# Performance work log

Measured on AMD Instinct MI355X. Metric: run time of the kernel, lower is better.

## Reference

```python
import jax, jax.numpy as jnp
import numpy as np

B, D, C = 16384, 1024, 2048

def setup_inputs() -> dict:
    key = jax.random.key(0)
    k1, k2 = jax.random.split(key)
    x = jax.random.normal(k1, (B, D), dtype=jnp.float32)
    # kaiming_normal_ with nonlinearity='relu': std = sqrt(2 / fan_in)
    W = jax.random.normal(k2, (C, D), dtype=jnp.float32) * jnp.sqrt(2.0 / D)
    return {"x": x, "W": W, "task_id": 0}

def reference(x, W, task_id):
    # Original: -(x[:, :, None] - W.T[None, :, :])**2 .mean(1)  -> [B, C]
    # Algebraic rewrite: -(||x||^2/D - 2*x.W^T/D + ||w||^2/D)
    d = jnp.asarray(x.shape[1], x.dtype)
    x2 = jnp.sum(x * x, axis=1, keepdims=True) / d          # [B, 1]
    w2 = jnp.sum(W * W, axis=1) / d                          # [C]
    cross = jnp.einsum('bd,cd->bc', x, W) * (2.0 / d)        # [B, C]
    return cross - x2 - w2[None, :]
```

## Files before the change

kernel.cpp:

```cpp
#include <hip/hip_runtime.h>
#include <hip/hip_bf16.h>
#include <stdint.h>

#define B_ROWS 16384
#define D_DIM  1024
#define C_DIM  2048

#define BM 128
#define BN 128
#define BK 64

typedef short bf16x8 __attribute__((ext_vector_type(8)));
typedef float f32x4  __attribute__((ext_vector_type(4)));

__global__ __launch_bounds__(256) void cvt_norm_all(
        const float* __restrict__ x, const float* __restrict__ W,
        ushort* __restrict__ xb, ushort* __restrict__ wb,
        float* __restrict__ x2, float* __restrict__ w2) {
    const int blk = blockIdx.x;
    const float* src; ushort* dst; float* norm; int row;
    if (blk < B_ROWS) { src = x; dst = xb; norm = x2; row = blk; }
    else              { src = W; dst = wb; norm = w2; row = blk - B_ROWS; }

    const int t = threadIdx.x;
    const float4 v = ((const float4*)(src + (size_t)row * D_DIM))[t];
    float s = v.x * v.x + v.y * v.y + v.z * v.z + v.w * v.w;

    ushort4 u;
    __hip_bfloat16 h;
    h = __float2bfloat16(v.x); u.x = *(const ushort*)&h;
    h = __float2bfloat16(v.y); u.y = *(const ushort*)&h;
    h = __float2bfloat16(v.z); u.z = *(const ushort*)&h;
    h = __float2bfloat16(v.w); u.w = *(const ushort*)&h;
    ((ushort4*)(dst + (size_t)row * D_DIM))[t] = u;

    #pragma unroll
    for (int o = 32; o > 0; o >>= 1) s += __shfl_down(s, o, 64);
    __shared__ float red[4];
    if ((t & 63) == 0) red[t >> 6] = s;
    __syncthreads();
    if (t == 0)
        norm[row] = (red[0] + red[1] + red[2] + red[3]) * (1.0f / (float)D_DIM);
}

__global__ __launch_bounds__(256) void gemm_epilogue(
        const ushort* __restrict__ xb, const ushort* __restrict__ wb,
        const float* __restrict__ x2, const float* __restrict__ w2,
        float* __restrict__ out) {
    __shared__ ushort As[BM * BK];
    __shared__ ushort Bs[BN * BK];

    const int tid  = threadIdx.x;
    const int lane = tid & 63;
    const int nT   = C_DIM / BN;
    const int per  = (B_ROWS / BM) * nT / 8;
    const int wid  = (blockIdx.x & 7) * per + (blockIdx.x >> 3);
    const int mBase = (wid / nT) * BM;
    const int nBase = (wid % nT) * BN;

    const int waveM = ((tid >> 6) >> 1) * 64;
    const int waveN = ((tid >> 6) & 1) * 64;

    f32x4 acc[4][4];
    #pragma unroll
    for (int mi = 0; mi < 4; ++mi)
        #pragma unroll
        for (int ni = 0; ni < 4; ++ni)
            acc[mi][ni] = (f32x4){0.f, 0.f, 0.f, 0.f};

    const ushort* aG = xb + (size_t)mBase * D_DIM;
    const ushort* bG = wb + (size_t)nBase * D_DIM;

    const int rsel = lane & 15;
    const int quad = lane >> 4;
    const int rk   = rsel & 7;

    for (int kt = 0; kt < D_DIM; kt += BK) {
        #pragma unroll
        for (int j = 0; j < 4; ++j) {
            const int c    = j * 256 + tid;
            const int row  = c >> 3;
            const int ksrc = (c & 7) ^ (row & 7);
            const int ldsb = (j * 256 + (tid & 192)) * 8;
            __builtin_amdgcn_global_load_lds(
                (const __attribute__((address_space(1))) void*)(aG + (size_t)row * D_DIM + kt + ksrc * 8),
                (__attribute__((address_space(3))) void*)(As + ldsb), 16, 0, 0);
            __builtin_amdgcn_global_load_lds(
                (const __attribute__((address_space(1))) void*)(bG + (size_t)row * D_DIM + kt + ksrc * 8),
                (__attribute__((address_space(3))) void*)(Bs + ldsb), 16, 0, 0);
        }
        __syncthreads();

        #pragma unroll
        for (int ks = 0; ks < 2; ++ks) {
            const int kph = ((ks * 4 + quad) ^ rk) * 8;
            bf16x8 a[4], b[4];
            #pragma unroll
            for (int mi = 0; mi < 4; ++mi)
                a[mi] = *(const bf16x8*)(As + (waveM + mi * 16 + rsel) * BK + kph);
            #pragma unroll
            for (int ni = 0; ni < 4; ++ni)
                b[ni] = *(const bf16x8*)(Bs + (waveN + ni * 16 + rsel) * BK + kph);
            #pragma unroll
            for (int mi = 0; mi < 4; ++mi)
                #pragma unroll
                for (int ni = 0; ni < 4; ++ni)
                    acc[mi][ni] = __builtin_amdgcn_mfma_f32_16x16x32_bf16(
                        a[mi], b[ni], acc[mi][ni], 0, 0, 0);
        }
        __syncthreads();
    }

    const float scale = 2.0f / (float)D_DIM;
    const int col0 = nBase + waveN + rsel;
    const int row0 = mBase + waveM + quad * 4;

    float x2r[4][4];
    #pragma unroll
    for (int mi = 0; mi < 4; ++mi)
        #pragma unroll
        for (int r = 0; r < 4; ++r)
            x2r[mi][r] = x2[row0 + mi * 16 + r];

    #pragma unroll
    for (int ni = 0; ni < 4; ++ni) {
        const int c = col0 + ni * 16;
        const float wc = w2[c];
        #pragma unroll
        for (int mi = 0; mi < 4; ++mi) {
            #pragma unroll
            for (int r = 0; r < 4; ++r) {
                const int rr = row0 + mi * 16 + r;
                out[(size_t)rr * C_DIM + c] = acc[mi][ni][r] * scale - x2r[mi][r] - wc;
            }
        }
    }
}

extern "C" void kernel_launch(void* const* d_in, const int* in_sizes, int n_in,
                              void* d_out, int out_size, void* d_ws, size_t ws_size,
                              hipStream_t stream) {
    const float* x = (const float*)d_in[0];
    const float* W = (const float*)d_in[1];
    float* out = (float*)d_out;

    char* ws = (char*)d_ws;
    ushort* xb = (ushort*)ws;
    ushort* wb = (ushort*)(ws + (size_t)B_ROWS * D_DIM * sizeof(ushort));
    float*  x2 = (float*)(ws + (size_t)(B_ROWS + C_DIM) * D_DIM * sizeof(ushort));
    float*  w2 = x2 + B_ROWS;

    cvt_norm_all<<<B_ROWS + C_DIM, 256, 0, stream>>>(x, W, xb, wb, x2, w2);
    gemm_epilogue<<<(B_ROWS / BM) * (C_DIM / BN), 256, 0, stream>>>(xb, wb, x2, w2, out);
}
```

Before: 267.3 us.

## Pre-pack operands into MFMA fragment layout and drop LDS from GEMM

The conversion kernel now writes x and W as bf16 in a tile-packed layout that matches the MFMA operand fragments, and accumulates row norms with atomics after a memset. The GEMM reads fragments straight from global memory into registers with double-buffered prefetch. This removes shared-memory staging and barriers. In exchange it loses LDS reuse across waves, so each wave fetches its own A/B fragments and L2 traffic goes up. It also adds an extra memset launch and atomic norm accumulation.

```diff
diff --git a/kernel.cpp b/kernel.cpp
--- a/kernel.cpp
+++ b/kernel.cpp
@@ -5,61 +5,65 @@
 #define B_ROWS 16384
 #define D_DIM  1024
 #define C_DIM  2048
-
-#define BM 128
-#define BN 128
-#define BK 64
+#define MT_TOT (B_ROWS / 16)
+#define NT_TOT (C_DIM  / 16)
+#define KT_TOT (D_DIM  / 32)
 
 typedef short bf16x8 __attribute__((ext_vector_type(8)));
 typedef float f32x4  __attribute__((ext_vector_type(4)));
 
-__global__ __launch_bounds__(256) void cvt_norm_all(
+__global__ __launch_bounds__(256) void pack_norm(
         const float* __restrict__ x, const float* __restrict__ W,
-        ushort* __restrict__ xb, ushort* __restrict__ wb,
+        ushort* __restrict__ Apk, ushort* __restrict__ Bpk,
         float* __restrict__ x2, float* __restrict__ w2) {
-    const int blk = blockIdx.x;
-    const float* src; ushort* dst; float* norm; int row;
-    if (blk < B_ROWS) { src = x; dst = xb; norm = x2; row = blk; }
-    else              { src = W; dst = wb; norm = w2; row = blk - B_ROWS; }
+    int chunk = blockIdx.x * 4 + (threadIdx.x >> 6);
+    const int lane = threadIdx.x & 63;
+    const int XCH = MT_TOT * KT_TOT;
+    const float* src; ushort* dst; float* norm;
+    if (chunk < XCH) { src = x; dst = Apk; norm = x2; }
+    else             { src = W; dst = Bpk; norm = w2; chunk -= XCH; }
+    const int tile = chunk >> 5;
+    const int kt   = chunk & 31;
 
-    const int t = threadIdx.x;
-    const float4 v = ((const float4*)(src + (size_t)row * D_DIM))[t];
-    float s = v.x * v.x + v.y * v.y + v.z * v.z + v.w * v.w;
+    const int row = tile * 16 + (lane & 15);
+    const int k0  = kt * 32 + (lane >> 4) * 8;
+    const float4 v0 = *(const float4*)(src + (size_t)row * D_DIM + k0);
+    const float4 v1 = *(const float4*)(src + (size_t)row * D_DIM + k0 + 4);
+    float s = v0.x*v0.x + v0.y*v0.y + v0.z*v0.z + v0.w*v0.w
+            + v1.x*v1.x + v1.y*v1.y + v1.z*v1.z + v1.w*v1.w;
 
-    ushort4 u;
-    __hip_bfloat16 h;
-    h = __float2bfloat16(v.x); u.x = *(const ushort*)&h;
-    h = __float2bfloat16(v.y); u.y = *(const ushort*)&h;
-    h = __float2bfloat16(v.z); u.z = *(const ushort*)&h;
-    h = __float2bfloat16(v.w); u.w = *(const ushort*)&h;
-    ((ushort4*)(dst + (size_t)row * D_DIM))[t] = u;
+    ushort u[8]; __hip_bfloat16 h;
+    h = __float2bfloat16(v0.x); u[0] = *(const ushort*)&h;
+    h = __float2bfloat16(v0.y); u[1] = *(const ushort*)&h;
+    h = __float2bfloat16(v0.z); u[2] = *(const ushort*)&h;
+    h = __float2bfloat16(v0.w); u[3] = *(const ushort*)&h;
+    h = __float2bfloat16(v1.x); u[4] = *(const ushort*)&h;
+    h = __float2bfloat16(v1.y); u[5] = *(const ushort*)&h;
+    h = __float2bfloat16(v1.z); u[6] = *(const ushort*)&h;
+    h = __float2bfloat16(v1.w); u[7] = *(const ushort*)&h;
+    *(bf16x8*)(dst + ((size_t)chunk * 64 + lane) * 8) = *(const bf16x8*)u;
 
-    #pragma unroll
-    for (int o = 32; o > 0; o >>= 1) s += __shfl_down(s, o, 64);
-    __shared__ float red[4];
-    if ((t & 63) == 0) red[t >> 6] = s;
-    __syncthreads();
-    if (t == 0)
-        norm[row] = (red[0] + red[1] + red[2] + red[3]) * (1.0f / (float)D_DIM);
+    s += __shfl_xor(s, 16, 64);
+    s += __shfl_xor(s, 32, 64);
+    if (lane < 16) atomicAdd(norm + tile * 16 + lane, s * (1.0f / (float)D_DIM));
 }
 
-__global__ __launch_bounds__(256) void gemm_epilogue(
-        const ushort* __restrict__ xb, const ushort* __restrict__ wb,
+__global__ __launch_bounds__(256, 3) void gemm_flat(
+        const ushort* __restrict__ Apk, const ushort* __restrict__ Bpk,
         const float* __restrict__ x2, const float* __restrict__ w2,
         float* __restrict__ out) {
-    __shared__ ushort As[BM * BK];
-    __shared__ ushort Bs[BN * BK];
-
     const int tid  = threadIdx.x;
     const int lane = tid & 63;
-    const int nT   = C_DIM / BN;
-    const int per  = (B_ROWS / BM) * nT / 8;
-    const int wid  = (blockIdx.x & 7) * per + (blockIdx.x >> 3);
-    const int mBase = (wid / nT) * BM;
-    const int nBase = (wid % nT) * BN;
+    const int wv   = tid >> 6;
 
-    const int waveM = ((tid >> 6) >> 1) * 64;
-    const int waveN = ((tid >> 6) & 1) * 64;
+    const int wid = (blockIdx.x & 7) * 256 + (blockIdx.x >> 3);
+    const int bm  = wid >> 4;
+    const int bn  = wid & 15;
+    const int mT0 = bm * 8 + (wv >> 1) * 4;
+    const int nT0 = bn * 8 + (wv & 1) * 4;
+
+    const ushort* aP = Apk + ((size_t)mT0 * KT_TOT) * 512 + lane * 8;
+    const ushort* bP = Bpk + ((size_t)nT0 * KT_TOT) * 512 + lane * 8;
 
     f32x4 acc[4][4];
     #pragma unroll
@@ -68,52 +72,47 @@
         for (int ni = 0; ni < 4; ++ni)
             acc[mi][ni] = (f32x4){0.f, 0.f, 0.f, 0.f};
 
-    const ushort* aG = xb + (size_t)mBase * D_DIM;
-    const ushort* bG = wb + (size_t)nBase * D_DIM;
+    bf16x8 aC[4], bC[4], aN[4], bN[4];
 
-    const int rsel = lane & 15;
-    const int quad = lane >> 4;
-    const int rk   = rsel & 7;
+    #pragma unroll
+    for (int i = 0; i < 4; ++i) {
+        aC[i] = *(const bf16x8*)(aP + i * (KT_TOT * 512));
+        bC[i] = *(const bf16x8*)(bP + i * (KT_TOT * 512));
+    }
 
-    for (int kt = 0; kt < D_DIM; kt += BK) {
+    #pragma unroll 4
+    for (int kt = 0; kt < KT_TOT; kt += 2) {
+        const int k1 = kt + 1;
+        const int k2 = (kt + 2 < KT_TOT) ? kt + 2 : KT_TOT - 1;
         #pragma unroll
-        for (int j = 0; j < 4; ++j) {
-            const int c    = j * 256 + tid;
-            const int row  = c >> 3;
-            const int ksrc = (c & 7) ^ (row & 7);
-            const int ldsb = (j * 256 + (tid & 192)) * 8;
-            __builtin_amdgcn_global_load_lds(
-                (const __attribute__((address_space(1))) void*)(aG + (size_t)row * D_DIM + kt + ksrc * 8),
-                (__attribute__((address_space(3))) void*)(As + ldsb), 16, 0, 0);
-            __builtin_amdgcn_global_load_lds(
-                (const __attribute__((address_space(1))) void*)(bG + (size_t)row * D_DIM + kt + ksrc * 8),
-                (__attribute__((address_space(3))) void*)(Bs + ldsb), 16, 0, 0);
+        for (int i = 0; i < 4; ++i) {
+            aN[i] = *(const bf16x8*)(aP + i * (KT_TOT * 512) + k1 * 512);
+            bN[i] = *(const bf16x8*)(bP + i * (KT_TOT * 512) + k1 * 512);
         }
-        __syncthreads();
-
         #pragma unroll
-        for (int ks = 0; ks < 2; ++ks) {
-            const int kph = ((ks * 4 + quad) ^ rk) * 8;
-            bf16x8 a[4], b[4];
-            #pragma unroll
-            for (int mi = 0; mi < 4; ++mi)
-                a[mi] = *(const bf16x8*)(As + (waveM + mi * 16 + rsel) * BK + kph);
+        for (int mi = 0; mi < 4; ++mi)
             #pragma unroll
             for (int ni = 0; ni < 4; ++ni)
-                b[ni] = *(const bf16x8*)(Bs + (waveN + ni * 16 + rsel) * BK + kph);
+                acc[mi][ni] = __builtin_amdgcn_mfma_f32_16x16x32_bf16(
+                    aC[mi], bC[ni], acc[mi][ni], 0, 0, 0);
+        #pragma unroll
+        for (int i = 0; i < 4; ++i) {
+            aC[i] = *(const bf16x8*)(aP + i * (KT_TOT * 512) + k2 * 512);
+            bC[i] = *(const bf16x8*)(bP + i * (KT_TOT * 512) + k2 * 512);
+        }
+        #pragma unroll
+        for (int mi = 0; mi < 4; ++mi)
             #pragma unroll
-            for (int mi = 0; mi < 4; ++mi)
-                #pragma unroll
-                for (int ni = 0; ni < 4; ++ni)
-                    acc[mi][ni] = __builtin_amdgcn_mfma_f32_16x16x32_bf16(
-                        a[mi], b[ni], acc[mi][ni], 0, 0, 0);
-        }
-        __syncthreads();
+            for (int ni = 0; ni < 4; ++ni)
+                acc[mi][ni] = __builtin_amdgcn_mfma_f32_16x16x32_bf16(
+                    aN[mi], bN[ni], acc[mi][ni], 0, 0, 0);
     }
 
     const float scale = 2.0f / (float)D_DIM;
-    const int col0 = nBase + waveN + rsel;
-    const int row0 = mBase + waveM + quad * 4;
+    const int rsel = lane & 15;
+    const int quad = lane >> 4;
+    const int row0 = mT0 * 16 + quad * 4;
+    const int col0 = nT0 * 16 + rsel;
 
     float x2r[4][4];
     #pragma unroll
@@ -145,11 +144,16 @@
     float* out = (float*)d_out;
 
     char* ws = (char*)d_ws;
-    ushort* xb = (ushort*)ws;
-    ushort* wb = (ushort*)(ws + (size_t)B_ROWS * D_DIM * sizeof(ushort));
-    float*  x2 = (float*)(ws + (size_t)(B_ROWS + C_DIM) * D_DIM * sizeof(ushort));
-    float*  w2 = x2 + B_ROWS;
+    ushort* Apk = (ushort*)ws;
+    ushort* Bpk = (ushort*)(ws + (size_t)B_ROWS * D_DIM * sizeof(ushort));
+    float*  x2  = (float*)(ws + (size_t)(B_ROWS + C_DIM) * D_DIM * sizeof(ushort));
+    float*  w2  = x2 + B_ROWS;
 
-    cvt_norm_all<<<B_ROWS + C_DIM, 256, 0, stream>>>(x, W, xb, wb, x2, w2);
-    gemm_epilogue<<<(B_ROWS / BM) * (C_DIM / BN), 256, 0, stream>>>(xb, wb, x2, w2, out);
+    hipMemsetAsync(x2, 0, (B_ROWS + C_DIM) * sizeof(float), stream);
+
+    pack_norm<<<(MT_TOT * KT_TOT + NT_TOT * KT_TOT) / 4, 256, 0, stream>>>(
+        x, W, Apk, Bpk, x2, w2);
+
+    gemm_flat<<<(B_ROWS / 128) * (C_DIM / 128), 256, 0, stream>>>(
+        Apk, Bpk, x2, w2, out);
 }
```

Result: slower. 301.2 us (+12.7%).
